# Kernel tuning notes

Measured on AMD Instinct MI355X. Metric: run time of the kernel, lower is better.

Reference implementation:

```python
import jax, jax.numpy as jnp
import numpy as np

B, K, N, D, E = 50000, 32, 200000, 256, 256


def setup_inputs() -> dict:
    key = jax.random.key(0)
    ks = jax.random.split(key, 8)
    return {
        "nodes": jax.random.randint(ks[0], (B,), 0, N),
        "neigh_idx": jax.random.randint(ks[1], (B, K), 0, N),
        "neigh_w": jax.random.uniform(ks[2], (B, K), dtype=jnp.float32),
        "features": jax.random.normal(ks[3], (N, D), dtype=jnp.float32),
        "W_init": jax.random.normal(ks[4], (D, E), dtype=jnp.float32) / np.sqrt(D),
        "b_init": jax.random.normal(ks[5], (E,), dtype=jnp.float32) * 0.01,
        "W_final": jax.random.normal(ks[6], (2 * D, E), dtype=jnp.float32) / np.sqrt(2 * D),
        "b_final": jax.random.normal(ks[7], (E,), dtype=jnp.float32) * 0.01,
    }


def reference(nodes, neigh_idx, neigh_w, features, W_init, b_init, W_final, b_final):
    # row-normalized neighbor weights (w /= sum(w) in the torch aggregator)
    w = neigh_w / jnp.sum(neigh_w, axis=1, keepdims=True)  # [B, K]
    # weighted mean of raw neighbor features (sparse mm in torch)
    neigh_feats = jnp.einsum("bk,bkd->bd", w, features[neigh_idx])  # [B, D]
    # self path: embedding lookup + init linear
    self_feats = features[nodes] @ W_init + b_init  # [B, E]
    combined = jnp.concatenate([self_feats, neigh_feats], axis=1)  # [B, 2D]
    z = combined @ W_final + b_final
    return z * jax.nn.sigmoid(z)  # swish
```

## Files before the change

### kernel.cpp

```cpp
#include <hip/hip_runtime.h>
#include <hip/hip_bf16.h>
#include <stdint.h>

#define NB 50000
#define KN 32
#define NN 200000
#define DD 256
#define EE 256

typedef unsigned short u16;
typedef __attribute__((ext_vector_type(8))) short bf16x8;
typedef __attribute__((ext_vector_type(4))) float f32x4;

static __device__ __forceinline__ u16 f2bf(float f) {
  __hip_bfloat16 h = __float2bfloat16(f);
  return *reinterpret_cast<u16*>(&h);
}
static __device__ __forceinline__ float bf2f(u16 u) {
  return __uint_as_float(((unsigned)u) << 16);
}

__global__ void wc_kernel(const float* __restrict__ Wi, const float* __restrict__ bi,
                          const float* __restrict__ Wf, const float* __restrict__ bf,
                          float* __restrict__ Wc, float* __restrict__ bc) {
  const int e = threadIdx.x;
  const int d = blockIdx.x;
  if (d < DD) {
    const float* wrow = Wi + (size_t)d * DD;
    float acc = 0.f;
    for (int t = 0; t < DD; ++t)
      acc = fmaf(wrow[t], Wf[(size_t)t * EE + e], acc);
    Wc[(size_t)d * EE + e] = acc;
  } else {
    float acc = bf[e];
    for (int t = 0; t < DD; ++t)
      acc = fmaf(bi[t], Wf[(size_t)t * EE + e], acc);
    bc[e] = acc;
  }
}

__global__ void wt_kernel(const float* __restrict__ Wc, const float* __restrict__ Wf,
                          u16* __restrict__ Bt) {
  const int e = blockIdx.x, d = threadIdx.x;
  Bt[(size_t)e * 512 + d]       = f2bf(Wc[(size_t)d * EE + e]);
  Bt[(size_t)e * 512 + 256 + d] = f2bf(Wf[(size_t)(DD + d) * EE + e]);
}

__global__ void cvt_kernel(const float* __restrict__ in, u16* __restrict__ out, int n4) {
  int i = blockIdx.x * blockDim.x + threadIdx.x;
  const int stride = gridDim.x * blockDim.x;
  for (; i < n4; i += stride) {
    float4 v = ((const float4*)in)[i];
    ushort4 o;
    o.x = f2bf(v.x); o.y = f2bf(v.y); o.z = f2bf(v.z); o.w = f2bf(v.w);
    ((ushort4*)out)[i] = o;
  }
}

template<int BF16FEAT>
__global__ void agg_kernel(const int* __restrict__ nodes,
                           const int* __restrict__ nidx,
                           const float* __restrict__ nw,
                           const void* __restrict__ featv,
                           u16* __restrict__ combined) {
  const int wave = threadIdx.x >> 6;
  const int lane = threadIdx.x & 63;
  const int b = blockIdx.x * 4 + wave;

  int idx = 0; float w = 0.f;
  if (lane < KN) {
    idx = nidx[(size_t)b * KN + lane];
    w   = nw[(size_t)b * KN + lane];
  }
  float s = w;
  #pragma unroll
  for (int off = 32; off >= 1; off >>= 1) s += __shfl_xor(s, off);
  const float inv = 1.f / s;

  float a0 = 0.f, a1 = 0.f, a2 = 0.f, a3 = 0.f;
  if (BF16FEAT) {
    const u16* f = (const u16*)featv;
    #pragma unroll
    for (int k = 0; k < KN; ++k) {
      const int   ik = __builtin_amdgcn_readlane(idx, k);
      const float wk = __uint_as_float(__builtin_amdgcn_readlane(__float_as_uint(w), k)) * inv;
      ushort4 v = *(const ushort4*)(f + (size_t)ik * DD + lane * 4);
      a0 = fmaf(wk, bf2f(v.x), a0);
      a1 = fmaf(wk, bf2f(v.y), a1);
      a2 = fmaf(wk, bf2f(v.z), a2);
      a3 = fmaf(wk, bf2f(v.w), a3);
    }
    const int node = nodes[b];
    ushort4 sv = *(const ushort4*)(f + (size_t)node * DD + lane * 4);
    ushort4 nv; nv.x = f2bf(a0); nv.y = f2bf(a1); nv.z = f2bf(a2); nv.w = f2bf(a3);
    *(ushort4*)(combined + (size_t)b * 512 + lane * 4) = sv;
    *(ushort4*)(combined + (size_t)b * 512 + 256 + lane * 4) = nv;
  } else {
    const float* f = (const float*)featv;
    #pragma unroll 8
    for (int k = 0; k < KN; ++k) {
      const int   ik = __builtin_amdgcn_readlane(idx, k);
      const float wk = __uint_as_float(__builtin_amdgcn_readlane(__float_as_uint(w), k)) * inv;
      float4 v = *(const float4*)(f + (size_t)ik * DD + lane * 4);
      a0 = fmaf(wk, v.x, a0);
      a1 = fmaf(wk, v.y, a1);
      a2 = fmaf(wk, v.z, a2);
      a3 = fmaf(wk, v.w, a3);
    }
    const int node = nodes[b];
    float4 sv = *(const float4*)(f + (size_t)node * DD + lane * 4);
    ushort4 so; so.x = f2bf(sv.x); so.y = f2bf(sv.y); so.z = f2bf(sv.z); so.w = f2bf(sv.w);
    ushort4 nv; nv.x = f2bf(a0);   nv.y = f2bf(a1);   nv.z = f2bf(a2);   nv.w = f2bf(a3);
    *(ushort4*)(combined + (size_t)b * 512 + lane * 4) = so;
    *(ushort4*)(combined + (size_t)b * 512 + 256 + lane * 4) = nv;
  }
}

#define BM 128
#define BN 64
#define BKK 32
#define LDT 72

__global__ __launch_bounds__(256) void gemm_kernel(const u16* __restrict__ A,
                                                   const u16* __restrict__ Bt,
                                                   const float* __restrict__ bc,
                                                   float* __restrict__ out, int M) {
  __shared__ u16 As[BM][LDT];
  __shared__ u16 Bs[BN][LDT];
  const int tid = threadIdx.x;
  const int wv = tid >> 6, lane = tid & 63;
  const int m0 = blockIdx.x * BM;
  const int n0 = blockIdx.y * BN;

  f32x4 acc[2][4];
  #pragma unroll
  for (int i = 0; i < 2; ++i)
    #pragma unroll
    for (int j = 0; j < 4; ++j) acc[i][j] = (f32x4){0.f, 0.f, 0.f, 0.f};

  const int ar0 = tid >> 2;
  const int as0 = tid & 3;
  int ga0 = m0 + ar0;      if (ga0 >= M) ga0 = M - 1;
  int ga1 = m0 + 64 + ar0; if (ga1 >= M) ga1 = M - 1;
  const u16* pA0 = A + (size_t)ga0 * 512 + as0 * 8;
  const u16* pA1 = A + (size_t)ga1 * 512 + as0 * 8;
  const u16* pB  = Bt + (size_t)(n0 + ar0) * 512 + as0 * 8;

  const int frow = lane & 15;
  const int fk = (lane >> 4) * 8;

  for (int k0 = 0; k0 < 512; k0 += BKK) {
    uint4 a0 = *(const uint4*)(pA0 + k0);
    uint4 a1 = *(const uint4*)(pA1 + k0);
    uint4 b0 = *(const uint4*)(pB + k0);
    __syncthreads();
    *(uint4*)&As[ar0][as0 * 8] = a0;
    *(uint4*)&As[64 + ar0][as0 * 8] = a1;
    *(uint4*)&Bs[ar0][as0 * 8] = b0;
    __syncthreads();

    bf16x8 af[2], bq[4];
    #pragma unroll
    for (int mf = 0; mf < 2; ++mf)
      af[mf] = *(const bf16x8*)&As[wv * 32 + mf * 16 + frow][fk];
    #pragma unroll
    for (int nf = 0; nf < 4; ++nf)
      bq[nf] = *(const bf16x8*)&Bs[nf * 16 + frow][fk];
    #pragma unroll
    for (int mf = 0; mf < 2; ++mf)
      #pragma unroll
      for (int nf = 0; nf < 4; ++nf)
        acc[mf][nf] = __builtin_amdgcn_mfma_f32_16x16x32_bf16(af[mf], bq[nf], acc[mf][nf], 0, 0, 0);
  }

  const int fcol = lane & 15;
  const int frq = (lane >> 4) * 4;
  #pragma unroll
  for (int nf = 0; nf < 4; ++nf) {
    const int col = n0 + nf * 16 + fcol;
    const float bias = bc[col];
    #pragma unroll
    for (int mf = 0; mf < 2; ++mf) {
      #pragma unroll
      for (int i = 0; i < 4; ++i) {
        const int row = m0 + wv * 32 + mf * 16 + frq + i;
        if (row < M) {
          const float z = acc[mf][nf][i] + bias;
          out[(size_t)row * EE + col] = z * (1.f / (1.f + __expf(-z)));
        }
      }
    }
  }
}

extern "C" void kernel_launch(void* const* d_in, const int* in_sizes, int n_in,
                              void* d_out, int out_size, void* d_ws, size_t ws_size,
                              hipStream_t stream) {
  const int*   nodes = (const int*)d_in[0];
  const int*   nidx  = (const int*)d_in[1];
  const float* nw    = (const float*)d_in[2];
  const float* feat  = (const float*)d_in[3];
  const float* Wi    = (const float*)d_in[4];
  const float* bi    = (const float*)d_in[5];
  const float* Wf    = (const float*)d_in[6];
  const float* bf    = (const float*)d_in[7];
  float* out = (float*)d_out;

  char* ws = (char*)d_ws;
  const size_t OFF_COMB = 0;
  const size_t OFF_WC   = 51200000;
  const size_t OFF_BC   = 51462144;
  const size_t OFF_BT   = 51463168;
  const size_t OFF_FB   = 51725312;
  const size_t NEED_BF16 = OFF_FB + (size_t)NN * DD * 2;

  u16*   combined = (u16*)(ws + OFF_COMB);
  float* Wc       = (float*)(ws + OFF_WC);
  float* bc       = (float*)(ws + OFF_BC);
  u16*   Bt       = (u16*)(ws + OFF_BT);
  u16*   fb       = (u16*)(ws + OFF_FB);

  const bool bf16feat = (ws_size >= NEED_BF16);

  wc_kernel<<<DD + 1, 256, 0, stream>>>(Wi, bi, Wf, bf, Wc, bc);
  wt_kernel<<<EE, 256, 0, stream>>>(Wc, Wf, Bt);

  if (bf16feat) {
    cvt_kernel<<<2048, 256, 0, stream>>>(feat, fb, NN * DD / 4);
    agg_kernel<1><<<NB / 4, 256, 0, stream>>>(nodes, nidx, nw, fb, combined);
  } else {
    agg_kernel<0><<<NB / 4, 256, 0, stream>>>(nodes, nidx, nw, feat, combined);
  }

  gemm_kernel<<<dim3((NB + BM - 1) / BM, EE / BN), 256, 0, stream>>>(combined, Bt, bc, out, NB);
}
```

Measured before the change: 498.3 us.

## Double-buffer GEMM with direct global-to-LDS loads, 128x128 tiles and swizzle

Rewrites the GEMM to use 128x128 tiles with double-buffered LDS staging via global_load_lds and an XOR-swizzled LDS layout, plus a block-id remap for locality. It also drops the fp32 fallback and always converts features to bf16. The intent is to overlap global loads with MFMA work and raise reuse per tile; the risk is that the unconditional bf16 buffer assumes enough workspace.

```diff
diff --git a/kernel.cpp b/kernel.cpp
--- a/kernel.cpp
+++ b/kernel.cpp
@@ -18,6 +18,21 @@
 }
 static __device__ __forceinline__ float bf2f(u16 u) {
   return __uint_as_float(((unsigned)u) << 16);
+}
+
+#if defined(__has_builtin)
+#if __has_builtin(__builtin_amdgcn_global_load_lds)
+#define HAVE_GLL 1
+#endif
+#endif
+
+static __device__ __forceinline__ void stage16(const u16* g, u16* l) {
+#ifdef HAVE_GLL
+  __builtin_amdgcn_global_load_lds((const __attribute__((address_space(1))) void*)g,
+                                   (__attribute__((address_space(3))) void*)l, 16, 0, 0);
+#else
+  *(uint4*)l = *(const uint4*)g;
+#endif
 }
 
 __global__ void wc_kernel(const float* __restrict__ Wi, const float* __restrict__ bi,
@@ -57,11 +72,10 @@
   }
 }
 
-template<int BF16FEAT>
 __global__ void agg_kernel(const int* __restrict__ nodes,
                            const int* __restrict__ nidx,
                            const float* __restrict__ nw,
-                           const void* __restrict__ featv,
+                           const u16* __restrict__ f,
                            u16* __restrict__ combined) {
   const int wave = threadIdx.x >> 6;
   const int lane = threadIdx.x & 63;
@@ -78,112 +92,116 @@
   const float inv = 1.f / s;
 
   float a0 = 0.f, a1 = 0.f, a2 = 0.f, a3 = 0.f;
-  if (BF16FEAT) {
-    const u16* f = (const u16*)featv;
-    #pragma unroll
-    for (int k = 0; k < KN; ++k) {
-      const int   ik = __builtin_amdgcn_readlane(idx, k);
-      const float wk = __uint_as_float(__builtin_amdgcn_readlane(__float_as_uint(w), k)) * inv;
-      ushort4 v = *(const ushort4*)(f + (size_t)ik * DD + lane * 4);
-      a0 = fmaf(wk, bf2f(v.x), a0);
-      a1 = fmaf(wk, bf2f(v.y), a1);
-      a2 = fmaf(wk, bf2f(v.z), a2);
-      a3 = fmaf(wk, bf2f(v.w), a3);
-    }
-    const int node = nodes[b];
-    ushort4 sv = *(const ushort4*)(f + (size_t)node * DD + lane * 4);
-    ushort4 nv; nv.x = f2bf(a0); nv.y = f2bf(a1); nv.z = f2bf(a2); nv.w = f2bf(a3);
-    *(ushort4*)(combined + (size_t)b * 512 + lane * 4) = sv;
-    *(ushort4*)(combined + (size_t)b * 512 + 256 + lane * 4) = nv;
-  } else {
-    const float* f = (const float*)featv;
-    #pragma unroll 8
-    for (int k = 0; k < KN; ++k) {
-      const int   ik = __builtin_amdgcn_readlane(idx, k);
-      const float wk = __uint_as_float(__builtin_amdgcn_readlane(__float_as_uint(w), k)) * inv;
-      float4 v = *(const float4*)(f + (size_t)ik * DD + lane * 4);
-      a0 = fmaf(wk, v.x, a0);
-      a1 = fmaf(wk, v.y, a1);
-      a2 = fmaf(wk, v.z, a2);
-      a3 = fmaf(wk, v.w, a3);
-    }
-    const int node = nodes[b];
-    float4 sv = *(const float4*)(f + (size_t)node * DD + lane * 4);
-    ushort4 so; so.x = f2bf(sv.x); so.y = f2bf(sv.y); so.z = f2bf(sv.z); so.w = f2bf(sv.w);
-    ushort4 nv; nv.x = f2bf(a0);   nv.y = f2bf(a1);   nv.z = f2bf(a2);   nv.w = f2bf(a3);
-    *(ushort4*)(combined + (size_t)b * 512 + lane * 4) = so;
-    *(ushort4*)(combined + (size_t)b * 512 + 256 + lane * 4) = nv;
-  }
+  #pragma unroll
+  for (int k = 0; k < KN; ++k) {
+    const int   ik = __builtin_amdgcn_readlane(idx, k);
+    const float wk = __uint_as_float(__builtin_amdgcn_readlane(__float_as_uint(w), k)) * inv;
+    ushort4 v = *(const ushort4*)(f + (size_t)ik * DD + lane * 4);
+    a0 = fmaf(wk, bf2f(v.x), a0);
+    a1 = fmaf(wk, bf2f(v.y), a1);
+    a2 = fmaf(wk, bf2f(v.z), a2);
+    a3 = fmaf(wk, bf2f(v.w), a3);
+  }
+  const int node = nodes[b];
+  ushort4 sv = *(const ushort4*)(f + (size_t)node * DD + lane * 4);
+  ushort4 nv; nv.x = f2bf(a0); nv.y = f2bf(a1); nv.z = f2bf(a2); nv.w = f2bf(a3);
+  *(ushort4*)(combined + (size_t)b * 512 + lane * 4) = sv;
+  *(ushort4*)(combined + (size_t)b * 512 + 256 + lane * 4) = nv;
 }
 
 #define BM 128
-#define BN 64
-#define BKK 32
-#define LDT 72
+#define BN 128
+#define BK 32
+#define NSTEP 16
+#define LROW 32
 
 __global__ __launch_bounds__(256) void gemm_kernel(const u16* __restrict__ A,
                                                    const u16* __restrict__ Bt,
                                                    const float* __restrict__ bc,
                                                    float* __restrict__ out, int M) {
-  __shared__ u16 As[BM][LDT];
-  __shared__ u16 Bs[BN][LDT];
+  __shared__ u16 sA[2][BM * LROW];
+  __shared__ u16 sB[2][BN * LROW];
   const int tid = threadIdx.x;
-  const int wv = tid >> 6, lane = tid & 63;
-  const int m0 = blockIdx.x * BM;
-  const int n0 = blockIdx.y * BN;
-
-  f32x4 acc[2][4];
-  #pragma unroll
-  for (int i = 0; i < 2; ++i)
+  const int l = tid & 63, wv = tid >> 6;
+  const int wm = wv >> 1, wn = wv & 1;
+
+  int id = blockIdx.x;
+  {
+    const int nwg = gridDim.x;
+    const int q = nwg >> 3, r = nwg & 7;
+    const int x = id & 7, p = id >> 3;
+    id = (x < r ? x * (q + 1) : r * (q + 1) + (x - r) * q) + p;
+  }
+  const int m0 = (id >> 1) * BM;
+  const int n0 = (id & 1) * BN;
+
+  const int srow  = l >> 2;
+  const int gslot = (l & 3) ^ ((l >> 3) & 3);
+  const int w0 = wv * 2;
+  int ar0 = m0 + w0 * 16 + srow;       if (ar0 >= M) ar0 = M - 1;
+  int ar1 = m0 + (w0 + 1) * 16 + srow; if (ar1 >= M) ar1 = M - 1;
+  const u16* gA0 = A + (size_t)ar0 * 512 + gslot * 8;
+  const u16* gA1 = A + (size_t)ar1 * 512 + gslot * 8;
+  const u16* gB0 = Bt + (size_t)(n0 + w0 * 16 + srow) * 512 + gslot * 8;
+  const u16* gB1 = Bt + (size_t)(n0 + (w0 + 1) * 16 + srow) * 512 + gslot * 8;
+  const int dst0 = w0 * 512 + l * 8;
+  const int dst1 = dst0 + 512;
+
+  const int fr = l & 15;
+  const int slotr = (l >> 4) ^ ((l >> 1) & 3);
+  int offA[4], offB[4];
+  #pragma unroll
+  for (int mf = 0; mf < 4; ++mf) offA[mf] = (wm * 64 + mf * 16 + fr) * LROW + slotr * 8;
+  #pragma unroll
+  for (int nf = 0; nf < 4; ++nf) offB[nf] = (wn * 64 + nf * 16 + fr) * LROW + slotr * 8;
+
+  f32x4 acc[4][4];
+  #pragma unroll
+  for (int i = 0; i < 4; ++i)
     #pragma unroll
     for (int j = 0; j < 4; ++j) acc[i][j] = (f32x4){0.f, 0.f, 0.f, 0.f};
 
-  const int ar0 = tid >> 2;
-  const int as0 = tid & 3;
-  int ga0 = m0 + ar0;      if (ga0 >= M) ga0 = M - 1;
-  int ga1 = m0 + 64 + ar0; if (ga1 >= M) ga1 = M - 1;
-  const u16* pA0 = A + (size_t)ga0 * 512 + as0 * 8;
-  const u16* pA1 = A + (size_t)ga1 * 512 + as0 * 8;
-  const u16* pB  = Bt + (size_t)(n0 + ar0) * 512 + as0 * 8;
-
-  const int frow = lane & 15;
-  const int fk = (lane >> 4) * 8;
-
-  for (int k0 = 0; k0 < 512; k0 += BKK) {
-    uint4 a0 = *(const uint4*)(pA0 + k0);
-    uint4 a1 = *(const uint4*)(pA1 + k0);
-    uint4 b0 = *(const uint4*)(pB + k0);
-    __syncthreads();
-    *(uint4*)&As[ar0][as0 * 8] = a0;
-    *(uint4*)&As[64 + ar0][as0 * 8] = a1;
-    *(uint4*)&Bs[ar0][as0 * 8] = b0;
-    __syncthreads();
-
-    bf16x8 af[2], bq[4];
-    #pragma unroll
-    for (int mf = 0; mf < 2; ++mf)
-      af[mf] = *(const bf16x8*)&As[wv * 32 + mf * 16 + frow][fk];
-    #pragma unroll
-    for (int nf = 0; nf < 4; ++nf)
-      bq[nf] = *(const bf16x8*)&Bs[nf * 16 + frow][fk];
-    #pragma unroll
-    for (int mf = 0; mf < 2; ++mf)
+  stage16(gA0, sA[0] + dst0);
+  stage16(gA1, sA[0] + dst1);
+  stage16(gB0, sB[0] + dst0);
+  stage16(gB1, sB[0] + dst1);
+  __syncthreads();
+
+  int cur = 0;
+  for (int t = 0; t < NSTEP; ++t) {
+    if (t + 1 < NSTEP) {
+      const int kn = (t + 1) * BK;
+      stage16(gA0 + kn, sA[cur ^ 1] + dst0);
+      stage16(gA1 + kn, sA[cur ^ 1] + dst1);
+      stage16(gB0 + kn, sB[cur ^ 1] + dst0);
+      stage16(gB1 + kn, sB[cur ^ 1] + dst1);
+    }
+    bf16x8 af[4], bq[4];
+    #pragma unroll
+    for (int mf = 0; mf < 4; ++mf) af[mf] = *(const bf16x8*)(sA[cur] + offA[mf]);
+    #pragma unroll
+    for (int nf = 0; nf < 4; ++nf) bq[nf] = *(const bf16x8*)(sB[cur] + offB[nf]);
+    #pragma unroll
+    for (int mf = 0; mf < 4; ++mf)
       #pragma unroll
       for (int nf = 0; nf < 4; ++nf)
         acc[mf][nf] = __builtin_amdgcn_mfma_f32_16x16x32_bf16(af[mf], bq[nf], acc[mf][nf], 0, 0, 0);
-  }
-
-  const int fcol = lane & 15;
-  const int frq = (lane >> 4) * 4;
+    __syncthreads();
+    cur ^= 1;
+  }
+
+  const int fcol = l & 15;
+  const int frq = (l >> 4) * 4;
   #pragma unroll
   for (int nf = 0; nf < 4; ++nf) {
-    const int col = n0 + nf * 16 + fcol;
+    const int col = n0 + wn * 64 + nf * 16 + fcol;
     const float bias = bc[col];
     #pragma unroll
-    for (int mf = 0; mf < 2; ++mf) {
+    for (int mf = 0; mf < 4; ++mf) {
+      const int rowb = m0 + wm * 64 + mf * 16 + frq;
       #pragma unroll
       for (int i = 0; i < 4; ++i) {
-        const int row = m0 + wv * 32 + mf * 16 + frq + i;
+        const int row = rowb + i;
         if (row < M) {
           const float z = acc[mf][nf][i] + bias;
           out[(size_t)row * EE + col] = z * (1.f / (1.f + __expf(-z)));
@@ -212,7 +230,6 @@
   const size_t OFF_BC   = 51462144;
   const size_t OFF_BT   = 51463168;
   const size_t OFF_FB   = 51725312;
-  const size_t NEED_BF16 = OFF_FB + (size_t)NN * DD * 2;
 
   u16*   combined = (u16*)(ws + OFF_COMB);
   float* Wc       = (float*)(ws + OFF_WC);
@@ -220,17 +237,11 @@
   u16*   Bt       = (u16*)(ws + OFF_BT);
   u16*   fb       = (u16*)(ws + OFF_FB);
 
-  const bool bf16feat = (ws_size >= NEED_BF16);
-
   wc_kernel<<<DD + 1, 256, 0, stream>>>(Wi, bi, Wf, bf, Wc, bc);
   wt_kernel<<<EE, 256, 0, stream>>>(Wc, Wf, Bt);
-
-  if (bf16feat) {
-    cvt_kernel<<<2048, 256, 0, stream>>>(feat, fb, NN * DD / 4);
-    agg_kernel<1><<<NB / 4, 256, 0, stream>>>(nodes, nidx, nw, fb, combined);
-  } else {
-    agg_kernel<0><<<NB / 4, 256, 0, stream>>>(nodes, nidx, nw, feat, combined);
-  }
-
-  gemm_kernel<<<dim3((NB + BM - 1) / BM, EE / BN), 256, 0, stream>>>(combined, Bt, bc, out, NB);
-}
+  cvt_kernel<<<2048, 256, 0, stream>>>(feat, fb, NN * DD / 4);
+  agg_kernel<<<NB / 4, 256, 0, stream>>>(nodes, nidx, nw, fb, combined);
+
+  const int mblocks = (NB + BM - 1) / BM;
+  gemm_kernel<<<mblocks * 2, 256, 0, stream>>>(combined, Bt, bc, out, NB);
+}
```

Result: no change. 503.1 us (+1.0%).

## Fuse neighbor aggregation with MFMA GEMM, keeping combined rows in shared memory

Applied to the files above, without the earlier changes.

Replaces the separate aggregation kernel and tiled GEMM with one kernel. Each 512-thread block gathers 64 rows into an XOR-swizzled LDS tile, with each wave handling two neighbors per step using 16-byte loads. It then runs the full-N MFMA GEMM, reading B fragments straight from global memory. This removes the 51 MB combined-buffer round trip and an extra launch. The cost is serialised gather-then-compute phases per block, uncached B loads, a 64 KB LDS tile that limits occupancy, and dropping the fp32 fallback when workspace is small.

```diff
diff --git a/kernel.cpp b/kernel.cpp
--- a/kernel.cpp
+++ b/kernel.cpp
@@ -16,8 +16,11 @@
   __hip_bfloat16 h = __float2bfloat16(f);
   return *reinterpret_cast<u16*>(&h);
 }
-static __device__ __forceinline__ float bf2f(u16 u) {
-  return __uint_as_float(((unsigned)u) << 16);
+static __device__ __forceinline__ float blo(unsigned u) {
+  return __uint_as_float(u << 16);
+}
+static __device__ __forceinline__ float bhi(unsigned u) {
+  return __uint_as_float(u & 0xffff0000u);
 }
 
 __global__ void wc_kernel(const float* __restrict__ Wi, const float* __restrict__ bi,
@@ -57,115 +60,93 @@
   }
 }
 
-template<int BF16FEAT>
-__global__ void agg_kernel(const int* __restrict__ nodes,
-                           const int* __restrict__ nidx,
-                           const float* __restrict__ nw,
-                           const void* __restrict__ featv,
-                           u16* __restrict__ combined) {
-  const int wave = threadIdx.x >> 6;
-  const int lane = threadIdx.x & 63;
-  const int b = blockIdx.x * 4 + wave;
-
-  int idx = 0; float w = 0.f;
-  if (lane < KN) {
-    idx = nidx[(size_t)b * KN + lane];
-    w   = nw[(size_t)b * KN + lane];
-  }
-  float s = w;
-  #pragma unroll
-  for (int off = 32; off >= 1; off >>= 1) s += __shfl_xor(s, off);
-  const float inv = 1.f / s;
-
-  float a0 = 0.f, a1 = 0.f, a2 = 0.f, a3 = 0.f;
-  if (BF16FEAT) {
-    const u16* f = (const u16*)featv;
-    #pragma unroll
-    for (int k = 0; k < KN; ++k) {
-      const int   ik = __builtin_amdgcn_readlane(idx, k);
-      const float wk = __uint_as_float(__builtin_amdgcn_readlane(__float_as_uint(w), k)) * inv;
-      ushort4 v = *(const ushort4*)(f + (size_t)ik * DD + lane * 4);
-      a0 = fmaf(wk, bf2f(v.x), a0);
-      a1 = fmaf(wk, bf2f(v.y), a1);
-      a2 = fmaf(wk, bf2f(v.z), a2);
-      a3 = fmaf(wk, bf2f(v.w), a3);
+#define BMF 64
+
+__global__ __launch_bounds__(512, 4) void fused_kernel(const int* __restrict__ nodes,
+                                                       const int* __restrict__ nidx,
+                                                       const float* __restrict__ nw,
+                                                       const u16* __restrict__ fb,
+                                                       const u16* __restrict__ Bt,
+                                                       const float* __restrict__ bc,
+                                                       float* __restrict__ out, int M) {
+  __shared__ u16 sA[BMF * 512];
+  const int tid = threadIdx.x;
+  const int l = tid & 63, wv = tid >> 6;
+  const int m0 = blockIdx.x * BMF;
+  const int h = l >> 5, j = l & 31;
+
+  for (int rr = 0; rr < 8; ++rr) {
+    const int r = wv * 8 + rr;
+    int b = m0 + r; if (b >= M) b = M - 1;
+
+    int   idxv = 0; float wgt = 0.f;
+    if (l < KN) {
+      idxv = nidx[(size_t)b * KN + l];
+      wgt  = nw[(size_t)b * KN + l];
+    }
+    float s = wgt;
+    #pragma unroll
+    for (int off = 32; off >= 1; off >>= 1) s += __shfl_xor(s, off);
+    const float inv = 1.f / s;
+
+    float a[8];
+    #pragma unroll
+    for (int i = 0; i < 8; ++i) a[i] = 0.f;
+
+    #pragma unroll
+    for (int kp = 0; kp < 16; ++kp) {
+      const int   ik0 = __builtin_amdgcn_readlane(idxv, 2 * kp);
+      const int   ik1 = __builtin_amdgcn_readlane(idxv, 2 * kp + 1);
+      const float w0  = __uint_as_float(__builtin_amdgcn_readlane(__float_as_uint(wgt), 2 * kp)) * inv;
+      const float w1  = __uint_as_float(__builtin_amdgcn_readlane(__float_as_uint(wgt), 2 * kp + 1)) * inv;
+      const int   ik  = h ? ik1 : ik0;
+      const float wk  = h ? w1 : w0;
+      const uint4 v = *(const uint4*)(fb + (size_t)ik * DD + j * 8);
+      a[0] = fmaf(wk, blo(v.x), a[0]); a[1] = fmaf(wk, bhi(v.x), a[1]);
+      a[2] = fmaf(wk, blo(v.y), a[2]); a[3] = fmaf(wk, bhi(v.y), a[3]);
+      a[4] = fmaf(wk, blo(v.z), a[4]); a[5] = fmaf(wk, bhi(v.z), a[5]);
+      a[6] = fmaf(wk, blo(v.w), a[6]); a[7] = fmaf(wk, bhi(v.w), a[7]);
+    }
+    #pragma unroll
+    for (int i = 0; i < 8; ++i) a[i] += __shfl_xor(a[i], 32);
+
+    const int swz = r & 7;
+    if (l < 32) {
+      uint4 p;
+      p.x = (unsigned)f2bf(a[0]) | ((unsigned)f2bf(a[1]) << 16);
+      p.y = (unsigned)f2bf(a[2]) | ((unsigned)f2bf(a[3]) << 16);
+      p.z = (unsigned)f2bf(a[4]) | ((unsigned)f2bf(a[5]) << 16);
+      p.w = (unsigned)f2bf(a[6]) | ((unsigned)f2bf(a[7]) << 16);
+      *(uint4*)&sA[r * 512 + (((32 + j) ^ swz) * 8)] = p;
     }
     const int node = nodes[b];
-    ushort4 sv = *(const ushort4*)(f + (size_t)node * DD + lane * 4);
-    ushort4 nv; nv.x = f2bf(a0); nv.y = f2bf(a1); nv.z = f2bf(a2); nv.w = f2bf(a3);
-    *(ushort4*)(combined + (size_t)b * 512 + lane * 4) = sv;
-    *(ushort4*)(combined + (size_t)b * 512 + 256 + lane * 4) = nv;
-  } else {
-    const float* f = (const float*)featv;
-    #pragma unroll 8
-    for (int k = 0; k < KN; ++k) {
-      const int   ik = __builtin_amdgcn_readlane(idx, k);
-      const float wk = __uint_as_float(__builtin_amdgcn_readlane(__float_as_uint(w), k)) * inv;
-      float4 v = *(const float4*)(f + (size_t)ik * DD + lane * 4);
-      a0 = fmaf(wk, v.x, a0);
-      a1 = fmaf(wk, v.y, a1);
-      a2 = fmaf(wk, v.z, a2);
-      a3 = fmaf(wk, v.w, a3);
-    }
-    const int node = nodes[b];
-    float4 sv = *(const float4*)(f + (size_t)node * DD + lane * 4);
-    ushort4 so; so.x = f2bf(sv.x); so.y = f2bf(sv.y); so.z = f2bf(sv.z); so.w = f2bf(sv.w);
-    ushort4 nv; nv.x = f2bf(a0);   nv.y = f2bf(a1);   nv.z = f2bf(a2);   nv.w = f2bf(a3);
-    *(ushort4*)(combined + (size_t)b * 512 + lane * 4) = so;
-    *(ushort4*)(combined + (size_t)b * 512 + 256 + lane * 4) = nv;
-  }
-}
-
-#define BM 128
-#define BN 64
-#define BKK 32
-#define LDT 72
-
-__global__ __launch_bounds__(256) void gemm_kernel(const u16* __restrict__ A,
-                                                   const u16* __restrict__ Bt,
-                                                   const float* __restrict__ bc,
-                                                   float* __restrict__ out, int M) {
-  __shared__ u16 As[BM][LDT];
-  __shared__ u16 Bs[BN][LDT];
-  const int tid = threadIdx.x;
-  const int wv = tid >> 6, lane = tid & 63;
-  const int m0 = blockIdx.x * BM;
-  const int n0 = blockIdx.y * BN;
+    const ushort4 sv = *(const ushort4*)(fb + (size_t)node * DD + l * 4);
+    *(ushort4*)&sA[r * 512 + (((l >> 1) ^ swz) * 8) + (l & 1) * 4] = sv;
+  }
+  __syncthreads();
+
+  const int wm = wv >> 2, wn = wv & 3;
+  const int fr = l & 15, kc = l >> 4;
 
   f32x4 acc[2][4];
   #pragma unroll
   for (int i = 0; i < 2; ++i)
     #pragma unroll
-    for (int j = 0; j < 4; ++j) acc[i][j] = (f32x4){0.f, 0.f, 0.f, 0.f};
-
-  const int ar0 = tid >> 2;
-  const int as0 = tid & 3;
-  int ga0 = m0 + ar0;      if (ga0 >= M) ga0 = M - 1;
-  int ga1 = m0 + 64 + ar0; if (ga1 >= M) ga1 = M - 1;
-  const u16* pA0 = A + (size_t)ga0 * 512 + as0 * 8;
-  const u16* pA1 = A + (size_t)ga1 * 512 + as0 * 8;
-  const u16* pB  = Bt + (size_t)(n0 + ar0) * 512 + as0 * 8;
-
-  const int frow = lane & 15;
-  const int fk = (lane >> 4) * 8;
-
-  for (int k0 = 0; k0 < 512; k0 += BKK) {
-    uint4 a0 = *(const uint4*)(pA0 + k0);
-    uint4 a1 = *(const uint4*)(pA1 + k0);
-    uint4 b0 = *(const uint4*)(pB + k0);
-    __syncthreads();
-    *(uint4*)&As[ar0][as0 * 8] = a0;
-    *(uint4*)&As[64 + ar0][as0 * 8] = a1;
-    *(uint4*)&Bs[ar0][as0 * 8] = b0;
-    __syncthreads();
-
+    for (int jn = 0; jn < 4; ++jn) acc[i][jn] = (f32x4){0.f, 0.f, 0.f, 0.f};
+
+  const u16* bbase = Bt + (size_t)(wn * 64 + fr) * 512 + kc * 8;
+
+  for (int k0 = 0; k0 < 512; k0 += 32) {
     bf16x8 af[2], bq[4];
     #pragma unroll
-    for (int mf = 0; mf < 2; ++mf)
-      af[mf] = *(const bf16x8*)&As[wv * 32 + mf * 16 + frow][fk];
+    for (int mf = 0; mf < 2; ++mf) {
+      const int r = wm * 32 + mf * 16 + fr;
+      const int slot = ((k0 >> 3) + kc) ^ (r & 7);
+      af[mf] = *(const bf16x8*)&sA[r * 512 + slot * 8];
+    }
     #pragma unroll
     for (int nf = 0; nf < 4; ++nf)
-      bq[nf] = *(const bf16x8*)&Bs[nf * 16 + frow][fk];
+      bq[nf] = *(const bf16x8*)(bbase + (size_t)nf * 16 * 512 + k0);
     #pragma unroll
     for (int mf = 0; mf < 2; ++mf)
       #pragma unroll
@@ -173,17 +154,18 @@
         acc[mf][nf] = __builtin_amdgcn_mfma_f32_16x16x32_bf16(af[mf], bq[nf], acc[mf][nf], 0, 0, 0);
   }
 
-  const int fcol = lane & 15;
-  const int frq = (lane >> 4) * 4;
+  const int fcol = l & 15;
+  const int frq = (l >> 4) * 4;
   #pragma unroll
   for (int nf = 0; nf < 4; ++nf) {
-    const int col = n0 + nf * 16 + fcol;
+    const int col = wn * 64 + nf * 16 + fcol;
     const float bias = bc[col];
     #pragma unroll
     for (int mf = 0; mf < 2; ++mf) {
+      const int rowb = m0 + wm * 32 + mf * 16 + frq;
       #pragma unroll
       for (int i = 0; i < 4; ++i) {
-        const int row = m0 + wv * 32 + mf * 16 + frq + i;
+        const int row = rowb + i;
         if (row < M) {
           const float z = acc[mf][nf][i] + bias;
           out[(size_t)row * EE + col] = z * (1.f / (1.f + __expf(-z)));
@@ -207,30 +189,20 @@
   float* out = (float*)d_out;
 
   char* ws = (char*)d_ws;
-  const size_t OFF_COMB = 0;
-  const size_t OFF_WC   = 51200000;
-  const size_t OFF_BC   = 51462144;
-  const size_t OFF_BT   = 51463168;
-  const size_t OFF_FB   = 51725312;
-  const size_t NEED_BF16 = OFF_FB + (size_t)NN * DD * 2;
-
-  u16*   combined = (u16*)(ws + OFF_COMB);
-  float* Wc       = (float*)(ws + OFF_WC);
-  float* bc       = (float*)(ws + OFF_BC);
-  u16*   Bt       = (u16*)(ws + OFF_BT);
-  u16*   fb       = (u16*)(ws + OFF_FB);
-
-  const bool bf16feat = (ws_size >= NEED_BF16);
+  const size_t OFF_WC = 0;
+  const size_t OFF_BC = 262144;
+  const size_t OFF_BT = 263168;
+  const size_t OFF_FB = 525312;
+
+  float* Wc = (float*)(ws + OFF_WC);
+  float* bc = (float*)(ws + OFF_BC);
+  u16*   Bt = (u16*)(ws + OFF_BT);
+  u16*   fb = (u16*)(ws + OFF_FB);
 
   wc_kernel<<<DD + 1, 256, 0, stream>>>(Wi, bi, Wf, bf, Wc, bc);
   wt_kernel<<<EE, 256, 0, stream>>>(Wc, Wf, Bt);
-
-  if (bf16feat) {
-    cvt_kernel<<<2048, 256, 0, stream>>>(feat, fb, NN * DD / 4);
-    agg_kernel<1><<<NB / 4, 256, 0, stream>>>(nodes, nidx, nw, fb, combined);
-  } else {
-    agg_kernel<0><<<NB / 4, 256, 0, stream>>>(nodes, nidx, nw, feat, combined);
-  }
-
-  gemm_kernel<<<dim3((NB + BM - 1) / BM, EE / BN), 256, 0, stream>>>(combined, Bt, bc, out, NB);
-}
+  cvt_kernel<<<2048, 256, 0, stream>>>(feat, fb, NN * DD / 4);
+
+  const int blocks = (NB + BMF - 1) / BMF;
+  fused_kernel<<<blocks, 512, 0, stream>>>(nodes, nidx, nw, fb, Bt, bc, out, NB);
+}
```

New measurement: 518.4 us. +4.0%, slower.
